# Kernel tuning notes

Measured on AMD Instinct MI355X. Metric: run time of the kernel, lower is better.

Reference implementation:

```python
import jax, jax.numpy as jnp
import numpy as np

B, N, DIM, H, DH = 16, 1024, 768, 12, 64
SCALE = DH ** -0.5


def setup_inputs() -> dict:
    key = jax.random.key(0)
    k1, k2, k3 = jax.random.split(key, 3)
    x = jax.random.normal(k1, (B, N, DIM), dtype=jnp.float32)
    W_qkv = jax.random.normal(k2, (DIM, 3 * H * DH), dtype=jnp.float32) * (DIM ** -0.5)
    W_out = jax.random.normal(k3, (H * DH, DIM), dtype=jnp.float32) * ((H * DH) ** -0.5)
    b_out = jnp.zeros((DIM,), dtype=jnp.float32)
    # perm = [0] + random shuffle of 1..N-1 (matches module's construction)
    rng = np.random.default_rng(0)
    perm = jnp.asarray(np.concatenate([[0], rng.permutation(np.arange(1, N))]), dtype=jnp.int32)
    return {"x": x, "W_qkv": W_qkv, "W_out": W_out, "b_out": b_out, "perm": perm}


def reference(x, W_qkv, W_out, b_out, perm):
    # QKV projection: [b, n, 3*h*d]
    qkv = jnp.einsum('bnd,de->bne', x, W_qkv)
    q, k, v = jnp.split(qkv, 3, axis=-1)
    # [b, n, h*d] -> [b, h, n, d]
    reshape = lambda t: t.reshape(B, N, H, DH).transpose(0, 2, 1, 3)
    q, k, v = reshape(q), reshape(k), reshape(v)
    # permute query rows
    q = q[:, :, perm]
    dots = jnp.einsum('bhqd,bhkd->bhqk', q, k) * SCALE
    attn = jax.nn.softmax(dots, axis=-1)
    out = jnp.einsum('bhqk,bhkd->bhqd', attn, v)
    out = out.transpose(0, 2, 1, 3).reshape(B, N, H * DH)
    return jnp.einsum('bne,ed->bnd', out, W_out) + b_out
```

## Files before the change

kernel.cpp:

```cpp
#include <hip/hip_runtime.h>
#include <hip/hip_bf16.h>


typedef __bf16 bf16x8 __attribute__((ext_vector_type(8)));
typedef __bf16 bf16x4 __attribute__((ext_vector_type(4)));
typedef float  f32x4  __attribute__((ext_vector_type(4)));

__device__ __forceinline__ f32x4 mfma16(bf16x8 a, bf16x8 b, f32x4 c) {
    return __builtin_amdgcn_mfma_f32_16x16x32_bf16(a, b, c, 0, 0, 0);
}

__device__ __forceinline__ void async16(const void* g, void* l) {
    __builtin_amdgcn_global_load_lds(
        (const __attribute__((address_space(1))) unsigned int*)g,
        (__attribute__((address_space(3))) unsigned int*)l,
        16, 0, 0);
}

__global__ void detect_dtype(const unsigned short* __restrict__ raw, int* __restrict__ flag) {
    __shared__ int cnt;
    if (threadIdx.x == 0) cnt = 0;
    __syncthreads();
    int local = 0;
    for (int i = threadIdx.x; i < 2048; i += 256) {
        unsigned e = (raw[i] >> 7) & 0xFFu;
        if (e >= 0xC0u) local++;
    }
    atomicAdd(&cnt, local);
    __syncthreads();
    if (threadIdx.x == 0) *flag = (cnt > 16) ? 1 : 0;
}

__global__ void convert_to_bf16(const void* __restrict__ src, __bf16* __restrict__ dst,
                                int n4, const int* __restrict__ flag) {
    const int f = *flag;
    int i = blockIdx.x * blockDim.x + threadIdx.x;
    const int stride = gridDim.x * blockDim.x;
    if (f) {
        const float4* s = (const float4*)src;
        for (; i < n4; i += stride) {
            float4 v = s[i];
            bf16x4 o;
            o[0] = (__bf16)v.x; o[1] = (__bf16)v.y;
            o[2] = (__bf16)v.z; o[3] = (__bf16)v.w;
            *(bf16x4*)&dst[(size_t)i * 4] = o;
        }
    } else {
        const ushort4* s = (const ushort4*)src;
        for (; i < n4; i += stride) *(ushort4*)&dst[(size_t)i * 4] = s[i];
    }
}

__global__ void transpose_dyn(const void* __restrict__ in, __bf16* __restrict__ out,
                              int R, int C, const int* __restrict__ flag) {
    __shared__ __bf16 tile[64][65];
    const int f = *flag;
    const int c0 = blockIdx.x * 64, r0 = blockIdx.y * 64;
    const int tx = threadIdx.x, ty = threadIdx.y;
#pragma unroll
    for (int k = 0; k < 16; ++k) {
        int r = ty + 4 * k;
        size_t idx = (size_t)(r0 + r) * C + c0 + tx;
        tile[r][tx] = f ? (__bf16)((const float*)in)[idx] : ((const __bf16*)in)[idx];
    }
    __syncthreads();
#pragma unroll
    for (int k = 0; k < 16; ++k) {
        int cc = ty + 4 * k;
        out[(size_t)(c0 + cc) * R + r0 + tx] = tile[tx][cc];
    }
}

#define GMFMA16()                                                       \
    acc[0][0] = mfma16(af0, bf0, acc[0][0]);                            \
    acc[0][1] = mfma16(af0, bf1, acc[0][1]);                            \
    acc[0][2] = mfma16(af0, bf2, acc[0][2]);                            \
    acc[0][3] = mfma16(af0, bf3, acc[0][3]);                            \
    acc[1][0] = mfma16(af1, bf0, acc[1][0]);                            \
    acc[1][1] = mfma16(af1, bf1, acc[1][1]);                            \
    acc[1][2] = mfma16(af1, bf2, acc[1][2]);                            \
    acc[1][3] = mfma16(af1, bf3, acc[1][3]);                            \
    acc[2][0] = mfma16(af2, bf0, acc[2][0]);                            \
    acc[2][1] = mfma16(af2, bf1, acc[2][1]);                            \
    acc[2][2] = mfma16(af2, bf2, acc[2][2]);                            \
    acc[2][3] = mfma16(af2, bf3, acc[2][3]);                            \
    acc[3][0] = mfma16(af3, bf0, acc[3][0]);                            \
    acc[3][1] = mfma16(af3, bf1, acc[3][1]);                            \
    acc[3][2] = mfma16(af3, bf2, acc[3][2]);                            \
    acc[3][3] = mfma16(af3, bf3, acc[3][3])

#define GTILE(RD, ST, DO_STAGE, DO_SYNC) do {                           \
    if (DO_STAGE) {                                                     \
        async16(gA0, smem + (ST) + stA0);                               \
        async16(gA1, smem + (ST) + stA1);                               \
        async16(gB0, smem + (ST) + 8192 + stA0);                        \
        async16(gB1, smem + (ST) + 8192 + stA1);                        \
        gA0 += 32; gA1 += 32; gB0 += 32; gB1 += 32;                     \
    }                                                                   \
    bf16x8 af0 = *(const bf16x8*)(smem + (RD) + aoff0);                 \
    bf16x8 af1 = *(const bf16x8*)(smem + (RD) + aoff1);                 \
    bf16x8 af2 = *(const bf16x8*)(smem + (RD) + aoff2);                 \
    bf16x8 af3 = *(const bf16x8*)(smem + (RD) + aoff3);                 \
    bf16x8 bf0 = *(const bf16x8*)(smem + (RD) + boff0);                 \
    bf16x8 bf1 = *(const bf16x8*)(smem + (RD) + boff1);                 \
    bf16x8 bf2 = *(const bf16x8*)(smem + (RD) + boff2);                 \
    bf16x8 bf3 = *(const bf16x8*)(smem + (RD) + boff3);                 \
    GMFMA16();                                                          \
    if (DO_SYNC) {                                                      \
        asm volatile("s_waitcnt vmcnt(0)" ::: "memory");                \
        __builtin_amdgcn_s_barrier();                                   \
    }                                                                   \
} while (0)

template <int MODE>
__global__ __launch_bounds__(256, 3)
void gemm_bt(const __bf16* __restrict__ A, int lda,
             const __bf16* __restrict__ Bt,
             const void* __restrict__ bias,
             void* __restrict__ Cout, int ldc,
             int K, const int* __restrict__ flag,
             __bf16* __restrict__ vt) {
    __shared__ __align__(16) char smem[32768];
    const int tid  = threadIdx.x;
    const int wid  = tid >> 6;
    const int lane = tid & 63;
    const int quad = lane >> 4;
    const int l15  = lane & 15;

    const int bm = blockIdx.x * 128;
    const int bn = blockIdx.y * 128;

    const int wm = (wid & 1) * 64;
    const int wn = (wid >> 1) * 64;
    const int srow  = lane >> 2;
    const int sslot = lane & 3;

    const int rA0 = wid * 16 + srow;
    const int rA1 = 64 + wid * 16 + srow;
    const __bf16* gA0 = A  + (size_t)(bm + rA0) * lda + ((sslot ^ ((rA0 >> 1) & 3)) << 3);
    const __bf16* gA1 = A  + (size_t)(bm + rA1) * lda + ((sslot ^ ((rA1 >> 1) & 3)) << 3);
    const __bf16* gB0 = Bt + (size_t)(bn + rA0) * K   + ((sslot ^ ((rA0 >> 1) & 3)) << 3);
    const __bf16* gB1 = Bt + (size_t)(bn + rA1) * K   + ((sslot ^ ((rA1 >> 1) & 3)) << 3);
    const int stA0 = (wid * 16) * 64;
    const int stA1 = (64 + wid * 16) * 64;

    const int rf0 = wm + 0 * 16 + l15, rf1 = wm + 1 * 16 + l15;
    const int rf2 = wm + 2 * 16 + l15, rf3 = wm + 3 * 16 + l15;
    const int aoff0 = rf0 * 64 + ((quad ^ ((rf0 >> 1) & 3)) * 16);
    const int aoff1 = rf1 * 64 + ((quad ^ ((rf1 >> 1) & 3)) * 16);
    const int aoff2 = rf2 * 64 + ((quad ^ ((rf2 >> 1) & 3)) * 16);
    const int aoff3 = rf3 * 64 + ((quad ^ ((rf3 >> 1) & 3)) * 16);
    const int rg0 = wn + 0 * 16 + l15, rg1 = wn + 1 * 16 + l15;
    const int rg2 = wn + 2 * 16 + l15, rg3 = wn + 3 * 16 + l15;
    const int boff0 = 8192 + rg0 * 64 + ((quad ^ ((rg0 >> 1) & 3)) * 16);
    const int boff1 = 8192 + rg1 * 64 + ((quad ^ ((rg1 >> 1) & 3)) * 16);
    const int boff2 = 8192 + rg2 * 64 + ((quad ^ ((rg2 >> 1) & 3)) * 16);
    const int boff3 = 8192 + rg3 * 64 + ((quad ^ ((rg3 >> 1) & 3)) * 16);

    f32x4 acc[4][4];
#pragma unroll
    for (int i = 0; i < 4; ++i)
#pragma unroll
        for (int j = 0; j < 4; ++j) acc[i][j] = (f32x4)0.0f;

    async16(gA0, smem + stA0);
    async16(gA1, smem + stA1);
    async16(gB0, smem + 8192 + stA0);
    async16(gB1, smem + 8192 + stA1);
    gA0 += 32; gA1 += 32; gB0 += 32; gB1 += 32;
    asm volatile("s_waitcnt vmcnt(0)" ::: "memory");
    __builtin_amdgcn_s_barrier();

    const int nkt = K >> 5;
#pragma unroll 1
    for (int kt = 0; kt < nkt; kt += 2) {
        const bool more = (kt + 2 < nkt);
        GTILE(0,     16384, true, true);
        GTILE(16384, 0,     more, more);
    }

    if (MODE == 0 && bn >= 1536) {
        const int bq = bm >> 10;
        const int n0 = (bm & 1023) + wm + quad * 4;
        const int colb = bn - 1536 + wn;
#pragma unroll
        for (int mi = 0; mi < 4; ++mi)
#pragma unroll
            for (int ni = 0; ni < 4; ++ni) {
                int col = colb + ni * 16 + l15;
                bf16x4 v;
                v[0] = (__bf16)acc[mi][ni][0];
                v[1] = (__bf16)acc[mi][ni][1];
                v[2] = (__bf16)acc[mi][ni][2];
                v[3] = (__bf16)acc[mi][ni][3];
                *(bf16x4*)&vt[((size_t)bq * 768 + col) * 1024 + n0 + mi * 16] = v;
            }
        return;
    }

    const int f = (MODE == 1) ? *flag : 0;
    if (MODE == 1) {
#pragma unroll
        for (int ni = 0; ni < 4; ++ni) {
            int col = bn + wn + ni * 16 + l15;
            float bv = f ? ((const float*)bias)[col] : (float)((const __bf16*)bias)[col];
#pragma unroll
            for (int mi = 0; mi < 4; ++mi)
#pragma unroll
                for (int rg = 0; rg < 4; ++rg) acc[mi][ni][rg] += bv;
        }
    }

    if (MODE == 0 || !f) {
        __bf16* cs = (__bf16*)smem;
#pragma unroll
        for (int c = 0; c < 4; ++c) {
            __syncthreads();
            if (wm == (c >> 1) * 64) {
                int mb = (c & 1) * 2;
#pragma unroll
                for (int mloc = 0; mloc < 2; ++mloc) {
                    int rowc = mloc * 16 + quad * 4;
#pragma unroll
                    for (int ni = 0; ni < 4; ++ni) {
                        int col = wn + ni * 16 + l15;
#pragma unroll
                        for (int rg = 0; rg < 4; ++rg)
                            cs[(rowc + rg) * 136 + col] = (__bf16)acc[mb + mloc][ni][rg];
                    }
                }
            }
            __syncthreads();
#pragma unroll
            for (int p = 0; p < 2; ++p) {
                int row  = p * 16 + (tid >> 4);
                int colc = tid & 15;
                bf16x8 v = *(const bf16x8*)&cs[row * 136 + colc * 8];
                *(bf16x8*)((__bf16*)Cout + (size_t)(bm + c * 32 + row) * ldc + bn + colc * 8) = v;
            }
        }
    } else {
        float* cs = (float*)smem;
#pragma unroll
        for (int c = 0; c < 8; ++c) {
            __syncthreads();
            if (wm == (c >> 2) * 64) {
                int mi = c & 3;
                int rowc = quad * 4;
#pragma unroll
                for (int ni = 0; ni < 4; ++ni) {
                    int col = wn + ni * 16 + l15;
#pragma unroll
                    for (int rg = 0; rg < 4; ++rg)
                        cs[(rowc + rg) * 132 + col] = acc[mi][ni][rg];
                }
            }
            __syncthreads();
#pragma unroll
            for (int p = 0; p < 2; ++p) {
                int row  = p * 8 + (tid >> 5);
                int colc = tid & 31;
                float4 v = *(const float4*)&cs[row * 132 + colc * 4];
                *(float4*)((float*)Cout + (size_t)(bm + c * 16 + row) * ldc + bn + colc * 4) = v;
            }
        }
    }
}

__global__ __launch_bounds__(256, 2)
void attn(const __bf16* qkv, const __bf16* __restrict__ vt,
          const int* __restrict__ perm, __bf16* O, int ldo) {
    __shared__ __align__(16) char smem[55296];
    __bf16* Qs = (__bf16*)smem;
    __bf16* Ps = (__bf16*)(smem + 32768);

    const int tid  = threadIdx.x;
    const int wid  = tid >> 6;
    const int lane = tid & 63;
    const int quad = lane >> 4;
    const int l15  = lane & 15;
    const int bh = blockIdx.x;
    const int q0 = blockIdx.y * 128;
    const int b = bh / 12, h = bh % 12;
    const size_t row_base = (size_t)b * 1024;
    const int qcol = h * 64;
    const int kcol = 768 + h * 64;
    const int srow8  = lane >> 3;
    const int sslot8 = lane & 7;
    __bf16* Pw = Ps + wid * (32 * 88);

#pragma unroll
    for (int is = 0; is < 4; ++is) {
        int r = is * 32 + wid * 8 + srow8;
        int gr = perm[q0 + r];
        int chunk = sslot8 ^ (r & 7);
        async16(qkv + (row_base + gr) * 2304 + qcol + chunk * 8,
                &Qs[(is * 32 + wid * 8) * 64]);
    }
    __syncthreads();

    bf16x8 qf[2][2];
#pragma unroll
    for (int mi = 0; mi < 2; ++mi) {
        int r = wid * 32 + mi * 16 + l15;
#pragma unroll
        for (int ks = 0; ks < 2; ++ks)
            qf[mi][ks] = *(const bf16x8*)&Qs[r * 64 + (((ks * 4 + quad) ^ (r & 7)) * 8)];
    }
    asm volatile("s_waitcnt lgkmcnt(0)" ::: "memory");
    __builtin_amdgcn_sched_barrier(0);
    __builtin_amdgcn_s_barrier();

    const int off0 = l15 * 64 + (((0 * 4 + quad) ^ (l15 & 7)) * 8);
    const int off1 = l15 * 64 + (((1 * 4 + quad) ^ (l15 & 7)) * 8);
    const int pwb  = l15 * 88 + quad * 4;
    const int pfb  = l15 * 88 + quad * 8;

    const int rK = wid * 8 + srow8;
    const int ck = sslot8 ^ (rK & 7);
    const __bf16* kg0 = qkv + (row_base + rK) * 2304 + kcol + ck * 8;
    const __bf16* kg1 = kg0 + (size_t)32 * 2304;
    const __bf16* vg0 = vt + ((size_t)bh * 64 + rK) * 1024 + ck * 8;
    const __bf16* vg1 = vg0 + (size_t)32 * 1024;

    f32x4 acco[2][4];
#pragma unroll
    for (int mi = 0; mi < 2; ++mi)
#pragma unroll
        for (int ni = 0; ni < 4; ++ni) acco[mi][ni] = (f32x4)0.0f;
    float lsum[2] = {0.0f, 0.0f};

    const float cfac = 0.125f * 1.44269504088896340736f;

#define ASTAGE(KB, VB) do {                                             \
        async16(kg0, smem + (KB) + wid * 1024);                         \
        async16(kg1, smem + (KB) + 4096 + wid * 1024);                  \
        async16(vg0, smem + (VB) + wid * 1024);                         \
        async16(vg1, smem + (VB) + 4096 + wid * 1024);                  \
        kg0 += (size_t)64 * 2304; kg1 += (size_t)64 * 2304;             \
        vg0 += 64; vg1 += 64;                                           \
    } while (0)

    auto compute = [&](const __bf16* Kb, const __bf16* Vb) {
#pragma unroll
        for (int half = 0; half < 2; ++half) {
            f32x4 accs[2][2];
#pragma unroll
            for (int ki = 0; ki < 2; ++ki)
#pragma unroll
                for (int mi = 0; mi < 2; ++mi) accs[ki][mi] = (f32x4)0.0f;
#pragma unroll
            for (int ks = 0; ks < 2; ++ks) {
                const int off = ks ? off1 : off0;
                bf16x8 kf0 = *(const bf16x8*)&Kb[(half * 2 + 0) * 1024 + off];
                bf16x8 kf1 = *(const bf16x8*)&Kb[(half * 2 + 1) * 1024 + off];
                accs[0][0] = mfma16(kf0, qf[0][ks], accs[0][0]);
                accs[0][1] = mfma16(kf0, qf[1][ks], accs[0][1]);
                accs[1][0] = mfma16(kf1, qf[0][ks], accs[1][0]);
                accs[1][1] = mfma16(kf1, qf[1][ks], accs[1][1]);
            }

#pragma unroll
            for (int ki = 0; ki < 2; ++ki)
#pragma unroll
                for (int mi = 0; mi < 2; ++mi) {
                    bf16x4 pk;
                    float s0 = __builtin_amdgcn_exp2f(accs[ki][mi][0] * cfac - 8.0f);
                    float s1 = __builtin_amdgcn_exp2f(accs[ki][mi][1] * cfac - 8.0f);
                    float s2 = __builtin_amdgcn_exp2f(accs[ki][mi][2] * cfac - 8.0f);
                    float s3 = __builtin_amdgcn_exp2f(accs[ki][mi][3] * cfac - 8.0f);
                    pk[0] = (__bf16)s0; pk[1] = (__bf16)s1;
                    pk[2] = (__bf16)s2; pk[3] = (__bf16)s3;
                    lsum[mi] += (s0 + s1) + (s2 + s3);
                    *(bf16x4*)&Pw[pwb + mi * 1408 + (half * 2 + ki) * 16] = pk;
                }

            {
                bf16x8 pf0 = *(const bf16x8*)&Pw[pfb + 0 * 1408 + half * 32];
                bf16x8 pf1 = *(const bf16x8*)&Pw[pfb + 1 * 1408 + half * 32];
                const int offv = half ? off1 : off0;
#pragma unroll
                for (int ni = 0; ni < 4; ++ni) {
                    bf16x8 vf = *(const bf16x8*)&Vb[ni * 1024 + offv];
                    acco[0][ni] = mfma16(pf0, vf, acco[0][ni]);
                    acco[1][ni] = mfma16(pf1, vf, acco[1][ni]);
                }
            }
        }
    };

    ASTAGE(0, 16384);

#pragma unroll 1
    for (int kt2 = 0; kt2 < 8; ++kt2) {
        asm volatile("s_waitcnt vmcnt(0)" ::: "memory");
        __builtin_amdgcn_s_barrier();
        ASTAGE(8192, 16384 + 8192);
        compute((const __bf16*)smem, (const __bf16*)(smem + 16384));
        asm volatile("s_waitcnt vmcnt(0)" ::: "memory");
        __builtin_amdgcn_s_barrier();
        if (kt2 < 7) ASTAGE(0, 16384);
        compute((const __bf16*)(smem + 8192), (const __bf16*)(smem + 16384 + 8192));
    }
#undef ASTAGE

#pragma unroll
    for (int off = 16; off < 64; off <<= 1) {
        lsum[0] += __shfl_xor(lsum[0], off, 64);
        lsum[1] += __shfl_xor(lsum[1], off, 64);
    }

#pragma unroll
    for (int mi = 0; mi < 2; ++mi) {
#pragma unroll
        for (int rg = 0; rg < 4; ++rg) {
            float inv = 1.0f / __shfl(lsum[mi], quad * 4 + rg, 64);
            int orow = q0 + wid * 32 + mi * 16 + quad * 4 + rg;
#pragma unroll
            for (int ni = 0; ni < 4; ++ni) {
                int ocol = h * 64 + ni * 16 + l15;
                O[(row_base + orow) * (size_t)ldo + ocol] = (__bf16)(acco[mi][ni][rg] * inv);
            }
        }
    }
}

extern "C" void kernel_launch(void* const* d_in, const int* in_sizes, int n_in,
                              void* d_out, int out_size, void* d_ws, size_t ws_size,
                              hipStream_t stream) {
    (void)in_sizes; (void)n_in; (void)out_size; (void)ws_size;
    const void* x_raw    = d_in[0];
    const void* Wqkv_raw = d_in[1];
    const void* Wout_raw = d_in[2];
    const void* bout_raw = d_in[3];
    const int*  perm     = (const int*)d_in[4];

    char* ws = (char*)d_ws;
    int*    flag = (int*)ws;
    __bf16* Xc   = (__bf16*)(ws + 256);
    __bf16* QKV  = (__bf16*)(ws + 25166080);
    __bf16* Vt   = (__bf16*)(ws + 100663552);
    __bf16* Wqt  = (__bf16*)(ws + 125829376);
    __bf16* Wot  = (__bf16*)(ws + 129368320);
    __bf16* Obuf = QKV + 1536;

    detect_dtype<<<1, 256, 0, stream>>>((const unsigned short*)x_raw, flag);
    convert_to_bf16<<<2048, 256, 0, stream>>>(x_raw, Xc, 16384 * 768 / 4, flag);
    transpose_dyn<<<dim3(36, 12), dim3(64, 4), 0, stream>>>(Wqkv_raw, Wqt, 768, 2304, flag);
    transpose_dyn<<<dim3(12, 12), dim3(64, 4), 0, stream>>>(Wout_raw, Wot, 768, 768, flag);
    gemm_bt<0><<<dim3(128, 18), 256, 0, stream>>>(Xc, 768, Wqt, nullptr, QKV, 2304, 768, nullptr, Vt);
    attn<<<dim3(192, 8), 256, 0, stream>>>(QKV, Vt, perm, Obuf, 2304);
    gemm_bt<1><<<dim3(128, 6), 256, 0, stream>>>(Obuf, 2304, Wot, bout_raw, d_out, 768, 768, flag, nullptr);
}
```

Before: 209.8 us.

## Triple-buffer GEMM K-loop with partial vmcnt waits

Grows the GEMM shared-memory staging from two to three buffers and issues two tiles of prefetch before the loop, waiting with vmcnt(4) so one tile's loads can stay in flight while another is computed. The barrier moves to the start of each tile step. The loop is hardcoded to 24 k-tiles (K=768), which drops the generic K handling, and the larger LDS footprint may reduce occupancy below the launch-bounds target of 3 blocks. The attention kernel's waits also gain lgkmcnt(0).

```diff
diff --git a/kernel.cpp b/kernel.cpp
--- a/kernel.cpp
+++ b/kernel.cpp
@@ -89,7 +89,12 @@
     acc[3][2] = mfma16(af3, bf2, acc[3][2]);                            \
     acc[3][3] = mfma16(af3, bf3, acc[3][3])
 
-#define GTILE(RD, ST, DO_STAGE, DO_SYNC) do {                           \
+#define GTILE(RD, ST, DO_STAGE, VMK) do {                               \
+    if ((VMK) == 4)                                                     \
+        asm volatile("s_waitcnt vmcnt(4) lgkmcnt(0)" ::: "memory");     \
+    else                                                                \
+        asm volatile("s_waitcnt vmcnt(0) lgkmcnt(0)" ::: "memory");     \
+    __builtin_amdgcn_s_barrier();                                       \
     if (DO_STAGE) {                                                     \
         async16(gA0, smem + (ST) + stA0);                               \
         async16(gA1, smem + (ST) + stA1);                               \
@@ -106,10 +111,6 @@
     bf16x8 bf2 = *(const bf16x8*)(smem + (RD) + boff2);                 \
     bf16x8 bf3 = *(const bf16x8*)(smem + (RD) + boff3);                 \
     GMFMA16();                                                          \
-    if (DO_SYNC) {                                                      \
-        asm volatile("s_waitcnt vmcnt(0)" ::: "memory");                \
-        __builtin_amdgcn_s_barrier();                                   \
-    }                                                                   \
 } while (0)
 
 template <int MODE>
@@ -120,7 +121,7 @@
              void* __restrict__ Cout, int ldc,
              int K, const int* __restrict__ flag,
              __bf16* __restrict__ vt) {
-    __shared__ __align__(16) char smem[32768];
+    __shared__ __align__(16) char smem[49152];
     const int tid  = threadIdx.x;
     const int wid  = tid >> 6;
     const int lane = tid & 63;
@@ -168,16 +169,21 @@
     async16(gB0, smem + 8192 + stA0);
     async16(gB1, smem + 8192 + stA1);
     gA0 += 32; gA1 += 32; gB0 += 32; gB1 += 32;
-    asm volatile("s_waitcnt vmcnt(0)" ::: "memory");
-    __builtin_amdgcn_s_barrier();
-
-    const int nkt = K >> 5;
+    async16(gA0, smem + 16384 + stA0);
+    async16(gA1, smem + 16384 + stA1);
+    async16(gB0, smem + 16384 + 8192 + stA0);
+    async16(gB1, smem + 16384 + 8192 + stA1);
+    gA0 += 32; gA1 += 32; gB0 += 32; gB1 += 32;
+
 #pragma unroll 1
-    for (int kt = 0; kt < nkt; kt += 2) {
-        const bool more = (kt + 2 < nkt);
-        GTILE(0,     16384, true, true);
-        GTILE(16384, 0,     more, more);
-    }
+    for (int g = 0; g < 7; ++g) {
+        GTILE(0,     32768, true, 4);
+        GTILE(16384, 0,     true, 4);
+        GTILE(32768, 16384, true, 4);
+    }
+    GTILE(0,     32768, true,  4);
+    GTILE(16384, 0,     false, 4);
+    GTILE(32768, 0,     false, 0);
 
     if (MODE == 0 && bn >= 1536) {
         const int bq = bm >> 10;
@@ -393,11 +399,11 @@
 
 #pragma unroll 1
     for (int kt2 = 0; kt2 < 8; ++kt2) {
-        asm volatile("s_waitcnt vmcnt(0)" ::: "memory");
+        asm volatile("s_waitcnt vmcnt(0) lgkmcnt(0)" ::: "memory");
         __builtin_amdgcn_s_barrier();
         ASTAGE(8192, 16384 + 8192);
         compute((const __bf16*)smem, (const __bf16*)(smem + 16384));
-        asm volatile("s_waitcnt vmcnt(0)" ::: "memory");
+        asm volatile("s_waitcnt vmcnt(0) lgkmcnt(0)" ::: "memory");
         __builtin_amdgcn_s_barrier();
         if (kt2 < 7) ASTAGE(0, 16384);
         compute((const __bf16*)(smem + 8192), (const __bf16*)(smem + 16384 + 8192));
```

Result: no change. 206.5 us (-1.6%).
